# Kernel optimization log

Hardware: AMD Instinct MI355X
Metric: run time of the kernel (lower is better)

The kernel has to match this reference:

```python
import jax, jax.numpy as jnp
import numpy as np

QMIN, QMAX = -128, 127

def make_accurate_lut():
    # lut[i, j] = signed8(j) * signed8(i) with indices taken as uint8 bit patterns
    v = np.arange(256)
    v[v >= 128] -= 256
    xx, yy = np.meshgrid(v, v)
    return jnp.asarray((xx * yy).astype(np.int32))

def setup_inputs() -> dict:
    key = jax.random.key(0)
    kx, kw = jax.random.split(key)
    B, N, M, K = 4, 512, 512, 256
    x = jax.random.normal(kx, (B, N, M), dtype=jnp.float32)
    w = jax.random.normal(kw, (K, M), dtype=jnp.float32)
    return {
        "x": x,
        "w": w,
        "lut": make_accurate_lut(),                       # [256,256] int32
        "x_scale": jnp.ones((1,), jnp.float32) * 0.03,    # per-tensor affine quant params
        "x_zero_point": jnp.zeros((1,), jnp.float32),
        "w_scale": jnp.ones((1,), jnp.float32) * 0.03,
        "w_zero_point": jnp.zeros((1,), jnp.float32),
    }

def _quantize(t, scale, zp):
    # affine quantize to signed int8 range, kept in int32 for indexing
    q = jnp.round(t / scale + zp)
    return jnp.clip(q, QMIN, QMAX).astype(jnp.int32)

def _lut_gemm(xq, wq, lut):
    # xq: [B,N,M] int32 in [-128,127]; wq: [K,M]; lut: [256,256]
    xi = jnp.mod(xq, 256)  # uint8 bit-pattern index
    wi = jnp.mod(wq, 256)
    # gather per-element products via the LUT, then accumulate over M
    prods = lut[xi[:, :, None, :], wi[None, None, :, :]]  # [B,N,K,M] int32
    return prods.sum(axis=-1)                             # [B,N,K] int32

def reference(x, w, lut, x_scale, x_zero_point, w_scale, w_zero_point):
    xs, xzp = x_scale.reshape(()), x_zero_point.reshape(())
    ws, wzp = w_scale.reshape(()), w_zero_point.reshape(())
    M = x.shape[-1]
    xq = _quantize(x, xs, xzp)           # [B,N,M]
    wq = _quantize(w, ws, wzp)           # [K,M]
    acc = _lut_gemm(xq, wq, lut).astype(jnp.float32)  # ~ sum_m xq*wq via LUT
    # affine zero-point correction: sum (xq-xzp)(wq-wzp)
    acc = (acc
           - wzp * jnp.sum(xq, axis=-1, keepdims=True).astype(jnp.float32)
           - xzp * jnp.sum(wq, axis=-1).astype(jnp.float32)[None, None, :]
           + jnp.float32(M) * xzp * wzp)
    return acc * xs * ws                 # dequantized output [B,N,K]
```

## Files before the change

kernel.cpp:

```cpp
#include <hip/hip_runtime.h>

constexpr int Mdim = 512;
constexpr int Kdim = 256;
constexpr int ROWS = 2048;
constexpr int TILE_R = 8;
constexpr int MW = Mdim / 4;

extern "C" __device__ int __ockl_sdot4(int, int, int, bool);
__device__ __forceinline__ int dot4(int a, int b, int c) {
    return __ockl_sdot4(a, b, c, false);
}

__device__ __forceinline__ int qz(float v, float scale, float zp) {
    float q = rintf(v / scale + zp);
    q = fminf(fmaxf(q, -128.0f), 127.0f);
    return (int)q;
}

__device__ __forceinline__ int pack4(int q0, int q1, int q2, int q3) {
    return (q0 & 255) | ((q1 & 255) << 8) | ((q2 & 255) << 16) | ((q3 & 255) << 24);
}

__global__ __launch_bounds__(64) void quant_w_kernel(
        const float* __restrict__ w,
        const float* __restrict__ w_scale, const float* __restrict__ w_zp,
        int* __restrict__ wq_t, int* __restrict__ wsum) {
    const int k = blockIdx.x;
    const int tid = threadIdx.x;
    const float s = w_scale[0], zp = w_zp[0];

    const float4* wrow = (const float4*)(w + (size_t)k * Mdim);
    float4 a = wrow[tid * 2];
    float4 b = wrow[tid * 2 + 1];

    int q0 = qz(a.x, s, zp), q1 = qz(a.y, s, zp), q2 = qz(a.z, s, zp), q3 = qz(a.w, s, zp);
    int q4 = qz(b.x, s, zp), q5 = qz(b.y, s, zp), q6 = qz(b.z, s, zp), q7 = qz(b.w, s, zp);

    int w0 = pack4(q0, q1, q2, q3);
    int w1 = pack4(q4, q5, q6, q7);

    const int wi0 = 2 * tid;
    const int quad = wi0 >> 2;
    const int sub = wi0 & 3;
    *(int2*)&wq_t[((size_t)quad * Kdim + k) * 4 + sub] = make_int2(w0, w1);

    int sum = q0 + q1 + q2 + q3 + q4 + q5 + q6 + q7;
    #pragma unroll
    for (int off = 32; off > 0; off >>= 1) sum += __shfl_down(sum, off);
    if (tid == 0) wsum[k] = sum;
}

__global__ __launch_bounds__(256) void lut_gemm_kernel(
        const float* __restrict__ x,
        const int* __restrict__ wq_t, const int* __restrict__ wsum,
        const float* __restrict__ x_scale, const float* __restrict__ x_zp,
        const float* __restrict__ w_scale, const float* __restrict__ w_zp,
        float* __restrict__ out) {
    __shared__ __align__(16) int x_lds[TILE_R * MW];
    __shared__ int xsum[TILE_R];

    const int t = threadIdx.x;
    const int r0 = blockIdx.x * TILE_R;

    if (t < TILE_R) xsum[t] = 0;
    __syncthreads();

    const float xs = x_scale[0], xzpf = x_zp[0];
    const float wsf = w_scale[0], wzpf = w_zp[0];

    const float4* xrow4 = (const float4*)(x + (size_t)r0 * Mdim);
    #pragma unroll
    for (int i = 0; i < 4; ++i) {
        const int wi = i * 256 + t;
        float4 f = xrow4[wi];
        int q0 = qz(f.x, xs, xzpf), q1 = qz(f.y, xs, xzpf);
        int q2 = qz(f.z, xs, xzpf), q3 = qz(f.w, xs, xzpf);
        x_lds[wi] = pack4(q0, q1, q2, q3);
        int s = q0 + q1 + q2 + q3;
        #pragma unroll
        for (int off = 32; off > 0; off >>= 1) s += __shfl_down(s, off);
        if ((t & 63) == 0) atomicAdd(&xsum[wi >> 7], s);
    }
    __syncthreads();

    const int k = t;
    int acc[TILE_R];
    #pragma unroll
    for (int r = 0; r < TILE_R; ++r) acc[r] = 0;

    const int4* wq4 = (const int4*)wq_t;
    #pragma unroll 4
    for (int q = 0; q < MW / 4; ++q) {
        const int4 wv = wq4[(size_t)q * Kdim + k];
        #pragma unroll
        for (int r = 0; r < TILE_R; ++r) {
            const int4 xv = *(const int4*)&x_lds[r * MW + q * 4];
            acc[r] = dot4(xv.x, wv.x, acc[r]);
            acc[r] = dot4(xv.y, wv.y, acc[r]);
            acc[r] = dot4(xv.z, wv.z, acc[r]);
            acc[r] = dot4(xv.w, wv.w, acc[r]);
        }
    }

    const float wsumk = (float)wsum[k];
    const float corr_const = (float)Mdim * xzpf * wzpf - xzpf * wsumk;
    const float oscale = xs * wsf;
    #pragma unroll
    for (int r = 0; r < TILE_R; ++r) {
        float a = (float)acc[r] - wzpf * (float)xsum[r] + corr_const;
        out[(size_t)(r0 + r) * Kdim + k] = a * oscale;
    }
}

extern "C" void kernel_launch(void* const* d_in, const int* in_sizes, int n_in,
                              void* d_out, int out_size, void* d_ws, size_t ws_size,
                              hipStream_t stream) {
    const float* x       = (const float*)d_in[0];
    const float* w       = (const float*)d_in[1];
    const float* x_scale = (const float*)d_in[3];
    const float* x_zp    = (const float*)d_in[4];
    const float* w_scale = (const float*)d_in[5];
    const float* w_zp    = (const float*)d_in[6];
    float* out = (float*)d_out;

    int* wq_t = (int*)d_ws;
    int* wsum = wq_t + Kdim * MW;

    quant_w_kernel<<<Kdim, 64, 0, stream>>>(w, w_scale, w_zp, wq_t, wsum);
    lut_gemm_kernel<<<ROWS / TILE_R, 256, 0, stream>>>(
        x, wq_t, wsum, x_scale, x_zp, w_scale, w_zp, out);
}
```

Measured before the change: 77.85 us.

## Pre-quantize x in a fused quant kernel and split-M register-resident GEMM

New measurement: 75.56 us. 1.03x faster.

```diff
diff --git a/kernel.cpp b/kernel.cpp
--- a/kernel.cpp
+++ b/kernel.cpp
@@ -3,8 +3,13 @@
 constexpr int Mdim = 512;
 constexpr int Kdim = 256;
 constexpr int ROWS = 2048;
-constexpr int TILE_R = 8;
-constexpr int MW = Mdim / 4;
+constexpr int MW   = Mdim / 4;
+constexpr int R_PB = 4;
+
+constexpr int XQ_OFF   = 0;
+constexpr int WQT_OFF  = 262144;
+constexpr int XSUM_OFF = 294912;
+constexpr int WSUM_OFF = 296960;
 
 extern "C" __device__ int __ockl_sdot4(int, int, int, bool);
 __device__ __forceinline__ int dot4(int a, int b, int c) {
@@ -21,94 +26,96 @@
     return (q0 & 255) | ((q1 & 255) << 8) | ((q2 & 255) << 16) | ((q3 & 255) << 24);
 }
 
-__global__ __launch_bounds__(64) void quant_w_kernel(
-        const float* __restrict__ w,
+__global__ __launch_bounds__(64) void quant_kernel(
+        const float* __restrict__ x, const float* __restrict__ w,
+        const float* __restrict__ x_scale, const float* __restrict__ x_zp,
         const float* __restrict__ w_scale, const float* __restrict__ w_zp,
-        int* __restrict__ wq_t, int* __restrict__ wsum) {
-    const int k = blockIdx.x;
+        int* __restrict__ ws) {
     const int tid = threadIdx.x;
-    const float s = w_scale[0], zp = w_zp[0];
+    const bool is_x = (blockIdx.x < ROWS);
+    const int row = is_x ? blockIdx.x : (blockIdx.x - ROWS);
+    const float s  = is_x ? x_scale[0] : w_scale[0];
+    const float zp = is_x ? x_zp[0]    : w_zp[0];
+    const float* src = (is_x ? x : w) + (size_t)row * Mdim;
 
-    const float4* wrow = (const float4*)(w + (size_t)k * Mdim);
-    float4 a = wrow[tid * 2];
-    float4 b = wrow[tid * 2 + 1];
+    const float4* src4 = (const float4*)src;
+    float4 a = src4[tid * 2];
+    float4 b = src4[tid * 2 + 1];
 
     int q0 = qz(a.x, s, zp), q1 = qz(a.y, s, zp), q2 = qz(a.z, s, zp), q3 = qz(a.w, s, zp);
     int q4 = qz(b.x, s, zp), q5 = qz(b.y, s, zp), q6 = qz(b.z, s, zp), q7 = qz(b.w, s, zp);
-
     int w0 = pack4(q0, q1, q2, q3);
     int w1 = pack4(q4, q5, q6, q7);
 
-    const int wi0 = 2 * tid;
-    const int quad = wi0 >> 2;
-    const int sub = wi0 & 3;
-    *(int2*)&wq_t[((size_t)quad * Kdim + k) * 4 + sub] = make_int2(w0, w1);
+    if (is_x) {
+        *(int2*)&ws[XQ_OFF + row * MW + 2 * tid] = make_int2(w0, w1);
+    } else {
+        const int wi0 = 2 * tid;
+        const int quad = wi0 >> 2;
+        const int sub  = wi0 & 3;
+        *(int2*)&ws[WQT_OFF + ((size_t)quad * Kdim + row) * 4 + sub] = make_int2(w0, w1);
+    }
 
     int sum = q0 + q1 + q2 + q3 + q4 + q5 + q6 + q7;
     #pragma unroll
     for (int off = 32; off > 0; off >>= 1) sum += __shfl_down(sum, off);
-    if (tid == 0) wsum[k] = sum;
+    if (tid == 0) ws[(is_x ? XSUM_OFF : WSUM_OFF) + row] = sum;
 }
 
-__global__ __launch_bounds__(256) void lut_gemm_kernel(
-        const float* __restrict__ x,
-        const int* __restrict__ wq_t, const int* __restrict__ wsum,
+__global__ __launch_bounds__(512, 4) void lut_gemm_kernel(
+        const int* __restrict__ ws,
         const float* __restrict__ x_scale, const float* __restrict__ x_zp,
         const float* __restrict__ w_scale, const float* __restrict__ w_zp,
         float* __restrict__ out) {
-    __shared__ __align__(16) int x_lds[TILE_R * MW];
-    __shared__ int xsum[TILE_R];
+    __shared__ int accs[R_PB][Kdim];
 
     const int t = threadIdx.x;
-    const int r0 = blockIdx.x * TILE_R;
+    const int k = t & (Kdim - 1);
+    const int hu = __builtin_amdgcn_readfirstlane(t >> 8);
+    const int r0 = blockIdx.x * R_PB;
 
-    if (t < TILE_R) xsum[t] = 0;
-    __syncthreads();
+    const int4* wq4 = (const int4*)&ws[WQT_OFF];
+    int4 wv[16];
+    #pragma unroll
+    for (int q = 0; q < 16; ++q)
+        wv[q] = wq4[(size_t)(hu * 16 + q) * Kdim + k];
 
-    const float xs = x_scale[0], xzpf = x_zp[0];
-    const float wsf = w_scale[0], wzpf = w_zp[0];
+    int acc[R_PB];
+    #pragma unroll
+    for (int r = 0; r < R_PB; ++r) acc[r] = 0;
 
-    const float4* xrow4 = (const float4*)(x + (size_t)r0 * Mdim);
+    const int4* xq4 = (const int4*)&ws[XQ_OFF];
     #pragma unroll
-    for (int i = 0; i < 4; ++i) {
-        const int wi = i * 256 + t;
-        float4 f = xrow4[wi];
-        int q0 = qz(f.x, xs, xzpf), q1 = qz(f.y, xs, xzpf);
-        int q2 = qz(f.z, xs, xzpf), q3 = qz(f.w, xs, xzpf);
-        x_lds[wi] = pack4(q0, q1, q2, q3);
-        int s = q0 + q1 + q2 + q3;
+    for (int r = 0; r < R_PB; ++r) {
+        const int4* xb = xq4 + (size_t)(r0 + r) * (MW / 4) + hu * 16;
         #pragma unroll
-        for (int off = 32; off > 0; off >>= 1) s += __shfl_down(s, off);
-        if ((t & 63) == 0) atomicAdd(&xsum[wi >> 7], s);
-    }
-    __syncthreads();
-
-    const int k = t;
-    int acc[TILE_R];
-    #pragma unroll
-    for (int r = 0; r < TILE_R; ++r) acc[r] = 0;
-
-    const int4* wq4 = (const int4*)wq_t;
-    #pragma unroll 4
-    for (int q = 0; q < MW / 4; ++q) {
-        const int4 wv = wq4[(size_t)q * Kdim + k];
-        #pragma unroll
-        for (int r = 0; r < TILE_R; ++r) {
-            const int4 xv = *(const int4*)&x_lds[r * MW + q * 4];
-            acc[r] = dot4(xv.x, wv.x, acc[r]);
-            acc[r] = dot4(xv.y, wv.y, acc[r]);
-            acc[r] = dot4(xv.z, wv.z, acc[r]);
-            acc[r] = dot4(xv.w, wv.w, acc[r]);
+        for (int q = 0; q < 16; ++q) {
+            int4 xv = xb[q];
+            acc[r] = dot4(xv.x, wv[q].x, acc[r]);
+            acc[r] = dot4(xv.y, wv[q].y, acc[r]);
+            acc[r] = dot4(xv.z, wv[q].z, acc[r]);
+            acc[r] = dot4(xv.w, wv[q].w, acc[r]);
         }
     }
 
-    const float wsumk = (float)wsum[k];
-    const float corr_const = (float)Mdim * xzpf * wzpf - xzpf * wsumk;
-    const float oscale = xs * wsf;
-    #pragma unroll
-    for (int r = 0; r < TILE_R; ++r) {
-        float a = (float)acc[r] - wzpf * (float)xsum[r] + corr_const;
-        out[(size_t)(r0 + r) * Kdim + k] = a * oscale;
+    if (hu == 1) {
+        #pragma unroll
+        for (int r = 0; r < R_PB; ++r) accs[r][k] = acc[r];
+    }
+    __syncthreads();
+    if (hu == 0) {
+        const float xs = x_scale[0], xzpf = x_zp[0];
+        const float wsf = w_scale[0], wzpf = w_zp[0];
+        const float wsumk = (float)ws[WSUM_OFF + k];
+        const float corr_const = (float)Mdim * xzpf * wzpf - xzpf * wsumk;
+        const float oscale = xs * wsf;
+        #pragma unroll
+        for (int r = 0; r < R_PB; ++r) {
+            int total = acc[r] + accs[r][k];
+            float xsumr = (float)ws[XSUM_OFF + (r0 + r)];
+            float v = (float)total - wzpf * xsumr + corr_const;
+            out[(size_t)(r0 + r) * Kdim + k] = v * oscale;
+        }
     }
 }
 
@@ -122,11 +129,8 @@
     const float* w_scale = (const float*)d_in[5];
     const float* w_zp    = (const float*)d_in[6];
     float* out = (float*)d_out;
+    int* ws = (int*)d_ws;
 
-    int* wq_t = (int*)d_ws;
-    int* wsum = wq_t + Kdim * MW;
-
-    quant_w_kernel<<<Kdim, 64, 0, stream>>>(w, w_scale, w_zp, wq_t, wsum);
-    lut_gemm_kernel<<<ROWS / TILE_R, 256, 0, stream>>>(
-        x, wq_t, wsum, x_scale, x_zp, w_scale, w_zp, out);
+    quant_kernel<<<ROWS + Kdim, 64, 0, stream>>>(x, w, x_scale, x_zp, w_scale, w_zp, ws);
+    lut_gemm_kernel<<<ROWS / R_PB, 512, 0, stream>>>(ws, x_scale, x_zp, w_scale, w_zp, out);
 }
```
